# Performance work log

Measured on AMD Instinct MI355X. Metric: run time of the kernel, lower is better.

## Reference

```python
import jax, jax.numpy as jnp
import numpy as np

NUM_NODES = 100000
NUM_EDGES = 3200000
NUM_GRAPHS = 64


def gcn_conv(x, edge_index, W, b):
    """PyG GCNConv: add self-loops, symmetric deg normalization, linear, scatter-add."""
    n = x.shape[0]
    loop = jnp.arange(n, dtype=edge_index.dtype)
    src = jnp.concatenate([edge_index[0], loop])  # message sources
    dst = jnp.concatenate([edge_index[1], loop])  # aggregation targets
    deg = jax.ops.segment_sum(jnp.ones_like(src, dtype=x.dtype), dst, num_segments=n)
    dis = jnp.where(deg > 0, jax.lax.rsqrt(jnp.maximum(deg, 1.0)), 0.0)
    norm = dis[src] * dis[dst]  # [E+N]
    h = x @ W  # linear transform first (small dims)
    msg = h[src] * norm[:, None]  # irregular gather
    out = jax.ops.segment_sum(msg, dst, num_segments=n)  # scatter-add
    return out + b


def setup_inputs() -> dict:
    key = jax.random.key(0)
    ks = jax.random.split(key, 12)
    x = jax.random.normal(ks[0], (NUM_NODES, 3), dtype=jnp.float32)
    edge_index = jax.random.randint(ks[1], (2, NUM_EDGES), 0, NUM_NODES, dtype=jnp.int64)
    batch = jnp.sort(jax.random.randint(ks[2], (NUM_NODES,), 0, NUM_GRAPHS, dtype=jnp.int64))
    def glorot(k, fan_in, fan_out):
        s = (6.0 / (fan_in + fan_out)) ** 0.5
        return jax.random.uniform(k, (fan_in, fan_out), jnp.float32, -s, s)
    return {
        'x': x, 'edge_index': edge_index, 'batch': batch,
        'W1': glorot(ks[3], 3, 32), 'b1': jnp.zeros((32,), jnp.float32),
        'W2': glorot(ks[4], 32, 16), 'b2': jnp.zeros((16,), jnp.float32),
        'W3': glorot(ks[5], 16, 8), 'b3': jnp.zeros((8,), jnp.float32),
        'Wf': glorot(ks[6], 8, 3), 'bf': jnp.zeros((3,), jnp.float32),
    }


def reference(x, edge_index, batch, W1, b1, W2, b2, W3, b3, Wf, bf):
    h = jax.nn.relu(gcn_conv(x, edge_index, W1, b1))
    h = jax.nn.relu(gcn_conv(h, edge_index, W2, b2))
    h = jax.nn.relu(gcn_conv(h, edge_index, W3, b3))
    # global mean pool over graphs
    sums = jax.ops.segment_sum(h, batch, num_segments=NUM_GRAPHS)
    cnts = jax.ops.segment_sum(jnp.ones((h.shape[0],), h.dtype), batch, num_segments=NUM_GRAPHS)
    pooled = sums / jnp.maximum(cnts, 1.0)[:, None]
    return pooled @ Wf + bf
```

## Files before the change

kernel.cpp:

```cpp
#include <hip/hip_runtime.h>

constexpr int N_NODES  = 100000;
constexpr int N_EDGES  = 3200000;
constexpr int N_GRAPHS = 64;

constexpr int BSHIFT  = 8;
constexpr int NBINS   = (N_NODES + 255) >> BSHIFT;
constexpr int BIN_CAP = 9216;
constexpr int EPB     = 8192;
constexpr int NB_BIN  = (N_EDGES + EPB - 1) / EPB;


__global__ __launch_bounds__(1024) void bin_kernel(
        const int* __restrict__ src, const int* __restrict__ dst,
        int* __restrict__ bin_cur, int2* __restrict__ binned) {
    __shared__ int hist[NBINS];
    __shared__ int base[NBINS];
    int tid = threadIdx.x;
    int e0 = blockIdx.x * EPB;
    int e1 = min(e0 + EPB, N_EDGES);
    for (int i = tid; i < NBINS; i += 1024) hist[i] = 0;
    __syncthreads();
    for (int e = e0 + tid; e < e1; e += 1024) atomicAdd(&hist[dst[e] >> BSHIFT], 1);
    __syncthreads();
    for (int i = tid; i < NBINS; i += 1024) {
        int h = hist[i];
        base[i] = h ? atomicAdd(&bin_cur[i], h) : 0;
    }
    __syncthreads();
    for (int i = tid; i < NBINS; i += 1024) hist[i] = 0;
    __syncthreads();
    for (int e = e0 + tid; e < e1; e += 1024) {
        int d = dst[e];
        int b = d >> BSHIFT;
        int r = base[b] + atomicAdd(&hist[b], 1);
        if (r < BIN_CAP) binned[(size_t)b * BIN_CAP + r] = make_int2(src[e], d);
    }
}

__global__ void binscan_kernel(const int* __restrict__ bin_cur, int* __restrict__ bin_base,
                               int* __restrict__ rowptr) {
    __shared__ int s[512];
    int t = threadIdx.x;
    int v = (t < NBINS) ? bin_cur[t] : 0;
    s[t] = v;
    __syncthreads();
    for (int o = 1; o < 512; o <<= 1) {
        int x = (t >= o) ? s[t - o] : 0;
        __syncthreads();
        s[t] += x;
        __syncthreads();
    }
    if (t < NBINS) bin_base[t] = s[t] - v;
    if (t == 0) rowptr[N_NODES] = N_EDGES;
}

__global__ __launch_bounds__(1024) void csrbuild_kernel(
        const int2* __restrict__ binned, const int* __restrict__ bin_cur,
        const int* __restrict__ bin_base, int* __restrict__ rowptr,
        float* __restrict__ dis, int* __restrict__ csr) {
    __shared__ int cnt[256];
    __shared__ int lofs[256];
    __shared__ int s[256];
    int b = blockIdx.x;
    int t = threadIdx.x;
    int size  = min(bin_cur[b], BIN_CAP);
    int gbase = bin_base[b];
    const int2* bp = binned + (size_t)b * BIN_CAP;
    if (t < 256) cnt[t] = 0;
    __syncthreads();
    for (int i = t; i < size; i += 1024) atomicAdd(&cnt[bp[i].y & 255], 1);
    __syncthreads();
    if (t < 256) {
        int n = (b << BSHIFT) + t;
        int deg = cnt[t];
        if (n < N_NODES) dis[n] = 1.0f / sqrtf((float)deg + 1.0f);
        s[t] = deg;
    }
    __syncthreads();
    for (int o = 1; o < 256; o <<= 1) {
        int x = 0;
        if (t < 256 && t >= o) x = s[t - o];
        __syncthreads();
        if (t < 256) s[t] += x;
        __syncthreads();
    }
    if (t < 256) {
        int n = (b << BSHIFT) + t;
        int deg = cnt[t];
        int excl = s[t] - deg;
        if (n < N_NODES) rowptr[n] = gbase + excl;
        lofs[t] = excl;
        cnt[t] = 0;
    }
    __syncthreads();
    for (int i = t; i < size; i += 1024) {
        int2 ed = bp[i];
        int ln = ed.y & 255;
        int r = atomicAdd(&cnt[ln], 1);
        csr[gbase + lofs[ln] + r] = ed.x;
    }
}


__global__ void pre1_kernel(const float* __restrict__ x, const float* __restrict__ dis,
                            float* __restrict__ xs) {
    int i = blockIdx.x * blockDim.x + threadIdx.x;
    if (i >= N_NODES) return;
    float d = dis[i];
    float4 v;
    v.x = x[(size_t)i * 3 + 0] * d;
    v.y = x[(size_t)i * 3 + 1] * d;
    v.z = x[(size_t)i * 3 + 2] * d;
    v.w = 0.f;
    *reinterpret_cast<float4*>(&xs[(size_t)i * 4]) = v;
}

template<int F, bool ADD_B, bool RELU>
__global__ void gather_kernel(const float* __restrict__ in, const int* __restrict__ rowptr,
                              const int* __restrict__ csr, const float* __restrict__ dis,
                              const float* __restrict__ b, float* __restrict__ out) {
    constexpr int GPB = 256 / F;
    int tid = threadIdx.x;
    int l = tid & (F - 1);
    int n = blockIdx.x * GPB + (tid / F);
    if (n >= N_NODES) return;
    int beg = rowptr[n], end = rowptr[n + 1];
    float a0 = in[(size_t)n * F + l];
    float a1 = 0.f, a2 = 0.f, a3 = 0.f;
    int k = beg;
    for (; k + 3 < end; k += 4) {
        int s0 = csr[k], s1 = csr[k + 1], s2 = csr[k + 2], s3 = csr[k + 3];
        a0 += in[(size_t)s0 * F + l];
        a1 += in[(size_t)s1 * F + l];
        a2 += in[(size_t)s2 * F + l];
        a3 += in[(size_t)s3 * F + l];
    }
    for (; k < end; ++k) a0 += in[(size_t)csr[k] * F + l];
    float v = ((a0 + a1) + (a2 + a3)) * dis[n];
    if (ADD_B) v += b[l];
    if (RELU) v = fmaxf(v, 0.f);
    out[(size_t)n * F + l] = v;
}

__global__ void lin1_kernel(const float* __restrict__ m, const float* __restrict__ W1,
                            const float* __restrict__ b1, float* __restrict__ h1) {
    int i = blockIdx.x * blockDim.x + threadIdx.x;
    if (i >= N_NODES) return;
    float4 mv = *reinterpret_cast<const float4*>(&m[(size_t)i * 4]);
#pragma unroll
    for (int f = 0; f < 32; ++f) {
        float s = b1[f];
        s = fmaf(mv.x, W1[0 * 32 + f], s);
        s = fmaf(mv.y, W1[1 * 32 + f], s);
        s = fmaf(mv.z, W1[2 * 32 + f], s);
        h1[(size_t)i * 32 + f] = fmaxf(s, 0.f);
    }
}

template<int FIN, int FOUT>
__global__ void lin_pre_kernel(const float* __restrict__ in, const float* __restrict__ W,
                               const float* __restrict__ dis, float* __restrict__ g) {
    int i = blockIdx.x * blockDim.x + threadIdx.x;
    if (i >= N_NODES) return;
    float xin[FIN];
#pragma unroll
    for (int k = 0; k < FIN; ++k) xin[k] = in[(size_t)i * FIN + k];
    float d = dis[i];
#pragma unroll
    for (int f = 0; f < FOUT; ++f) {
        float s = 0.f;
#pragma unroll
        for (int k = 0; k < FIN; ++k) s = fmaf(xin[k], W[k * FOUT + f], s);
        g[(size_t)i * FOUT + f] = s * d;
    }
}


__global__ void pool_kernel(const float* __restrict__ h, const int* __restrict__ batch,
                            float* __restrict__ pool) {
    __shared__ float lsum[N_GRAPHS * 8];
    __shared__ float lcnt[N_GRAPHS];
    int tid = threadIdx.x;
    for (int j = tid; j < N_GRAPHS * 8; j += blockDim.x) lsum[j] = 0.f;
    for (int j = tid; j < N_GRAPHS; j += blockDim.x) lcnt[j] = 0.f;
    __syncthreads();
    int i = blockIdx.x * blockDim.x + tid;
    if (i < N_NODES) {
        int gm = batch[i];
        const float4* hp = reinterpret_cast<const float4*>(&h[(size_t)i * 8]);
        float4 a = hp[0], bq = hp[1];
        atomicAdd(&lsum[gm * 8 + 0], a.x);
        atomicAdd(&lsum[gm * 8 + 1], a.y);
        atomicAdd(&lsum[gm * 8 + 2], a.z);
        atomicAdd(&lsum[gm * 8 + 3], a.w);
        atomicAdd(&lsum[gm * 8 + 4], bq.x);
        atomicAdd(&lsum[gm * 8 + 5], bq.y);
        atomicAdd(&lsum[gm * 8 + 6], bq.z);
        atomicAdd(&lsum[gm * 8 + 7], bq.w);
        atomicAdd(&lcnt[gm], 1.0f);
    }
    __syncthreads();
    for (int idx = tid; idx < N_GRAPHS * 9; idx += blockDim.x) {
        int gm = idx / 9, j = idx % 9;
        if (lcnt[gm] != 0.f) {
            if (j < 8) atomicAdd(&pool[gm * 8 + j], lsum[gm * 8 + j]);
            else       atomicAdd(&pool[512 + gm], lcnt[gm]);
        }
    }
}

__global__ void final_kernel(const float* __restrict__ pool, const float* __restrict__ Wf,
                             const float* __restrict__ bf, float* __restrict__ out) {
    int t = threadIdx.x;
    if (t >= N_GRAPHS * 3) return;
    int gm = t / 3, c = t % 3;
    float cnt = fmaxf(pool[512 + gm], 1.0f);
    float s = 0.f;
#pragma unroll
    for (int f = 0; f < 8; ++f) s = fmaf(pool[gm * 8 + f] / cnt, Wf[f * 3 + c], s);
    out[t] = s + bf[c];
}


extern "C" void kernel_launch(void* const* d_in, const int* in_sizes, int n_in,
                              void* d_out, int out_size, void* d_ws, size_t ws_size,
                              hipStream_t stream) {
    const float* x     = (const float*)d_in[0];
    const int*   ei    = (const int*)d_in[1];
    const int*   batch = (const int*)d_in[2];
    const float* W1 = (const float*)d_in[3];
    const float* b1 = (const float*)d_in[4];
    const float* W2 = (const float*)d_in[5];
    const float* b2 = (const float*)d_in[6];
    const float* W3 = (const float*)d_in[7];
    const float* b3 = (const float*)d_in[8];
    const float* Wf = (const float*)d_in[9];
    const float* bf = (const float*)d_in[10];

    const int* src = ei;
    const int* dst = ei + N_EDGES;

    const int N = N_NODES, E = N_EDGES;

    int*   bin_cur  = (int*)d_ws;
    int*   bin_base = bin_cur + NBINS;
    int*   rowptr   = bin_base + NBINS;
    float* dis      = (float*)(rowptr + N + 2);
    int*   csr      = (int*)(dis + N);
    int2*  binned   = (int2*)(csr + E);
    float* xs       = (float*)binned;
    float* m        = xs + (size_t)4 * N;
    float* h1       = m + (size_t)4 * N;
    float* g        = h1 + (size_t)32 * N;
    float* h2       = g + (size_t)16 * N;
    float* pool     = (float*)(binned + (size_t)NBINS * BIN_CAP);
    float* h3       = xs;

    const int B = 256;
    const int NB_N = (N + B - 1) / B;

    hipMemsetAsync(bin_cur, 0, NBINS * sizeof(int), stream);
    hipMemsetAsync(pool, 0, N_GRAPHS * 9 * sizeof(float), stream);

    bin_kernel<<<NB_BIN, 1024, 0, stream>>>(src, dst, bin_cur, binned);
    binscan_kernel<<<1, 512, 0, stream>>>(bin_cur, bin_base, rowptr);
    csrbuild_kernel<<<NBINS, 1024, 0, stream>>>(binned, bin_cur, bin_base, rowptr, dis, csr);

    pre1_kernel<<<NB_N, B, 0, stream>>>(x, dis, xs);
    gather_kernel<4, false, false><<<(N + 63) / 64, B, 0, stream>>>(xs, rowptr, csr, dis, b1, m);
    lin1_kernel<<<NB_N, B, 0, stream>>>(m, W1, b1, h1);

    lin_pre_kernel<32, 16><<<NB_N, B, 0, stream>>>(h1, W2, dis, g);
    gather_kernel<16, true, true><<<(N + 15) / 16, B, 0, stream>>>(g, rowptr, csr, dis, b2, h2);

    lin_pre_kernel<16, 8><<<NB_N, B, 0, stream>>>(h2, W3, dis, g);
    gather_kernel<8, true, true><<<(N + 31) / 32, B, 0, stream>>>(g, rowptr, csr, dis, b3, h3);

    pool_kernel<<<NB_N, B, 0, stream>>>(h3, batch, pool);
    final_kernel<<<1, 256, 0, stream>>>(pool, Wf, bf, (float*)d_out);
}
```

Before: 202.9 us.

## Pack binned edges into single ints and use finer 128-node bins

Each binned edge is now one 32-bit word, holding the local destination (7 bits) and the source index (17 bits), instead of an int2. This halves the memory traffic of the intermediate binned buffer. Bins shrink to 128 nodes, which gives more and smaller csrbuild blocks of 512 threads. The binning kernel now runs a fixed 512 blocks and keeps destination indices in registers between its two passes, so it reads dst only once. The packing depends on node ids fitting in 17 bits, and the per-bin capacity of 4608 must hold the random-graph bin sizes.

```diff
diff --git a/kernel.cpp b/kernel.cpp
--- a/kernel.cpp
+++ b/kernel.cpp
@@ -4,48 +4,67 @@
 constexpr int N_EDGES  = 3200000;
 constexpr int N_GRAPHS = 64;
 
-constexpr int BSHIFT  = 8;
-constexpr int NBINS   = (N_NODES + 255) >> BSHIFT;
-constexpr int BIN_CAP = 9216;
-constexpr int EPB     = 8192;
-constexpr int NB_BIN  = (N_EDGES + EPB - 1) / EPB;
+constexpr int BSHIFT  = 7;
+constexpr int BMASK   = 127;
+constexpr int NBINS   = (N_NODES + BMASK) >> BSHIFT;
+constexpr int BIN_CAP = 4608;
+constexpr int SRC_BITS = 17;
+constexpr int SRC_MASK = (1 << SRC_BITS) - 1;
+
+constexpr int NB_BIN  = 512;
+constexpr int EPB     = N_EDGES / NB_BIN;
+constexpr int EPT     = (EPB + 1023) / 1024;
 
 
 __global__ __launch_bounds__(1024) void bin_kernel(
         const int* __restrict__ src, const int* __restrict__ dst,
-        int* __restrict__ bin_cur, int2* __restrict__ binned) {
+        int* __restrict__ bin_cur, int* __restrict__ binned) {
     __shared__ int hist[NBINS];
     __shared__ int base[NBINS];
     int tid = threadIdx.x;
     int e0 = blockIdx.x * EPB;
-    int e1 = min(e0 + EPB, N_EDGES);
-    for (int i = tid; i < NBINS; i += 1024) hist[i] = 0;
-    __syncthreads();
-    for (int e = e0 + tid; e < e1; e += 1024) atomicAdd(&hist[dst[e] >> BSHIFT], 1);
-    __syncthreads();
-    for (int i = tid; i < NBINS; i += 1024) {
-        int h = hist[i];
-        base[i] = h ? atomicAdd(&bin_cur[i], h) : 0;
-    }
-    __syncthreads();
-    for (int i = tid; i < NBINS; i += 1024) hist[i] = 0;
-    __syncthreads();
-    for (int e = e0 + tid; e < e1; e += 1024) {
-        int d = dst[e];
-        int b = d >> BSHIFT;
-        int r = base[b] + atomicAdd(&hist[b], 1);
-        if (r < BIN_CAP) binned[(size_t)b * BIN_CAP + r] = make_int2(src[e], d);
-    }
-}
-
-__global__ void binscan_kernel(const int* __restrict__ bin_cur, int* __restrict__ bin_base,
-                               int* __restrict__ rowptr) {
-    __shared__ int s[512];
+    int e1 = e0 + EPB;
+    if (tid < NBINS) hist[tid] = 0;
+    __syncthreads();
+    int dc[EPT];
+#pragma unroll
+    for (int k = 0; k < EPT; ++k) {
+        int e = e0 + tid + k * 1024;
+        if (e < e1) {
+            int d = dst[e];
+            dc[k] = d;
+            atomicAdd(&hist[d >> BSHIFT], 1);
+        }
+    }
+    __syncthreads();
+    if (tid < NBINS) {
+        int h = hist[tid];
+        base[tid] = h ? atomicAdd(&bin_cur[tid], h) : 0;
+        hist[tid] = 0;
+    }
+    __syncthreads();
+#pragma unroll
+    for (int k = 0; k < EPT; ++k) {
+        int e = e0 + tid + k * 1024;
+        if (e < e1) {
+            int d = dc[k];
+            int b = d >> BSHIFT;
+            int r = base[b] + atomicAdd(&hist[b], 1);
+            if (r < BIN_CAP)
+                binned[(size_t)b * BIN_CAP + r] = ((d & BMASK) << SRC_BITS) | src[e];
+        }
+    }
+}
+
+__global__ __launch_bounds__(1024) void binscan_kernel(
+        const int* __restrict__ bin_cur, int* __restrict__ bin_base,
+        int* __restrict__ rowptr) {
+    __shared__ int s[1024];
     int t = threadIdx.x;
     int v = (t < NBINS) ? bin_cur[t] : 0;
     s[t] = v;
     __syncthreads();
-    for (int o = 1; o < 512; o <<= 1) {
+    for (int o = 1; o < 1024; o <<= 1) {
         int x = (t >= o) ? s[t - o] : 0;
         __syncthreads();
         s[t] += x;
@@ -55,50 +74,49 @@
     if (t == 0) rowptr[N_NODES] = N_EDGES;
 }
 
-__global__ __launch_bounds__(1024) void csrbuild_kernel(
-        const int2* __restrict__ binned, const int* __restrict__ bin_cur,
+__global__ __launch_bounds__(512) void csrbuild_kernel(
+        const int* __restrict__ binned, const int* __restrict__ bin_cur,
         const int* __restrict__ bin_base, int* __restrict__ rowptr,
         float* __restrict__ dis, int* __restrict__ csr) {
-    __shared__ int cnt[256];
-    __shared__ int lofs[256];
-    __shared__ int s[256];
+    __shared__ int cnt[128];
+    __shared__ int lofs[128];
+    __shared__ int s[128];
     int b = blockIdx.x;
     int t = threadIdx.x;
     int size  = min(bin_cur[b], BIN_CAP);
     int gbase = bin_base[b];
-    const int2* bp = binned + (size_t)b * BIN_CAP;
-    if (t < 256) cnt[t] = 0;
-    __syncthreads();
-    for (int i = t; i < size; i += 1024) atomicAdd(&cnt[bp[i].y & 255], 1);
-    __syncthreads();
-    if (t < 256) {
+    const int* bp = binned + (size_t)b * BIN_CAP;
+    if (t < 128) cnt[t] = 0;
+    __syncthreads();
+    for (int i = t; i < size; i += 512) atomicAdd(&cnt[bp[i] >> SRC_BITS], 1);
+    __syncthreads();
+    if (t < 128) {
         int n = (b << BSHIFT) + t;
         int deg = cnt[t];
         if (n < N_NODES) dis[n] = 1.0f / sqrtf((float)deg + 1.0f);
         s[t] = deg;
     }
     __syncthreads();
-    for (int o = 1; o < 256; o <<= 1) {
+    for (int o = 1; o < 128; o <<= 1) {
         int x = 0;
-        if (t < 256 && t >= o) x = s[t - o];
+        if (t < 128 && t >= o) x = s[t - o];
         __syncthreads();
-        if (t < 256) s[t] += x;
+        if (t < 128) s[t] += x;
         __syncthreads();
     }
-    if (t < 256) {
+    if (t < 128) {
         int n = (b << BSHIFT) + t;
-        int deg = cnt[t];
-        int excl = s[t] - deg;
+        int excl = s[t] - cnt[t];
         if (n < N_NODES) rowptr[n] = gbase + excl;
         lofs[t] = excl;
         cnt[t] = 0;
     }
     __syncthreads();
-    for (int i = t; i < size; i += 1024) {
-        int2 ed = bp[i];
-        int ln = ed.y & 255;
+    for (int i = t; i < size; i += 512) {
+        int p = bp[i];
+        int ln = p >> SRC_BITS;
         int r = atomicAdd(&cnt[ln], 1);
-        csr[gbase + lofs[ln] + r] = ed.x;
+        csr[gbase + lofs[ln] + r] = p & SRC_MASK;
     }
 }
 
@@ -248,13 +266,13 @@
     int*   rowptr   = bin_base + NBINS;
     float* dis      = (float*)(rowptr + N + 2);
     int*   csr      = (int*)(dis + N);
-    int2*  binned   = (int2*)(csr + E);
+    int*   binned   = csr + E;
     float* xs       = (float*)binned;
     float* m        = xs + (size_t)4 * N;
     float* h1       = m + (size_t)4 * N;
     float* g        = h1 + (size_t)32 * N;
     float* h2       = g + (size_t)16 * N;
-    float* pool     = (float*)(binned + (size_t)NBINS * BIN_CAP);
+    float* pool     = h2 + (size_t)16 * N;
     float* h3       = xs;
 
     const int B = 256;
@@ -264,8 +282,8 @@
     hipMemsetAsync(pool, 0, N_GRAPHS * 9 * sizeof(float), stream);
 
     bin_kernel<<<NB_BIN, 1024, 0, stream>>>(src, dst, bin_cur, binned);
-    binscan_kernel<<<1, 512, 0, stream>>>(bin_cur, bin_base, rowptr);
-    csrbuild_kernel<<<NBINS, 1024, 0, stream>>>(binned, bin_cur, bin_base, rowptr, dis, csr);
+    binscan_kernel<<<1, 1024, 0, stream>>>(bin_cur, bin_base, rowptr);
+    csrbuild_kernel<<<NBINS, 512, 0, stream>>>(binned, bin_cur, bin_base, rowptr, dis, csr);
 
     pre1_kernel<<<NB_N, B, 0, stream>>>(x, dis, xs);
     gather_kernel<4, false, false><<<(N + 63) / 64, B, 0, stream>>>(xs, rowptr, csr, dis, b1, m);
```

Result: slower. 217.9 us (+7.4%).
